# Optimization experiments

Measured on AMD Instinct MI355X. Metric: run time of the kernel, lower is better.

## Reference

```python
import jax, jax.numpy as jnp
import numpy as np

B, N, D, H = 2, 512, 384, 12
SQK, SV, PQ, PV = 16, 16, 4, 8
SCALE = 1.0 / np.sqrt(SQK + 4 * PQ)  # attention_scale, point_pair_dim=4
EPS = 1e-12


def setup_inputs() -> dict:
    key = jax.random.key(0)
    ks = jax.random.split(key, 10)

    def w(k, fan_in, fan_out):
        return (jax.random.normal(k, (fan_in, fan_out), jnp.float32) / np.sqrt(fan_in))

    return {
        "hidden": jax.random.normal(ks[0], (B, N, D), jnp.float32),
        "xyz": jax.random.normal(ks[1], (B, N, 3), jnp.float32),
        "W_qk": w(ks[2], D, 2 * H * SQK), "b_qk": jnp.zeros((2 * H * SQK,), jnp.float32),
        "W_vs": w(ks[3], D, H * SV), "b_vs": jnp.zeros((H * SV,), jnp.float32),
        "W_so": w(ks[4], H * SV, D), "b_so": jnp.zeros((D,), jnp.float32),
        "W_pqk": w(ks[5], D, H * PQ * 3), "b_pqk": jnp.zeros((H * PQ * 3,), jnp.float32),
        "W_pv": w(ks[6], D, H * PV * 3), "b_pv": jnp.zeros((H * PV * 3,), jnp.float32),
        "W_po": w(ks[7], H * PV * 3, D), "b_po": jnp.zeros((D,), jnp.float32),
        "W_fp": w(ks[8], 2 * D, D), "b_fp": jnp.zeros((D,), jnp.float32),
    }


def reference(hidden, xyz, W_qk, b_qk, W_vs, b_vs, W_so, b_so,
              W_pqk, b_pqk, W_pv, b_pv, W_po, b_po, W_fp, b_fp):
    # scalar q/k/v (note: heads are NOT split in the attention matmuls, per source)
    qk = hidden @ W_qk + b_qk                       # [B,N,2*H*SQK]
    q_s, k_s = jnp.split(qk, 2, axis=-1)            # [B,N,H*SQK] each
    v_s = hidden @ W_vs + b_vs                      # [B,N,H*SV]

    # points; k_points = q_points in source
    qp = (hidden @ W_pqk + b_pqk).reshape(B, N, H, PQ, 3)
    vp = hidden @ W_pv + b_pv                       # [B,N,H*PV*3]

    scalar_attn = jnp.einsum('bid,bjd->bij', q_s, k_s)  # [B,N,N]

    # fused pairwise point features: dist(q_i, k_j) + sum of 3 cosine components
    # = dist + cos_sim, per (head, point); avoid materializing [B,N,N,H,P,3].
    dot = jnp.einsum('bihpc,bjhpc->bijhp', qp, qp)      # [B,N,N,H,PQ]
    n2 = jnp.sum(qp * qp, axis=-1)                      # [B,N,H,PQ]
    d2 = n2[:, :, None] + n2[:, None] - 2.0 * dot
    dist = jnp.sqrt(jnp.maximum(d2, 0.0) + EPS)
    nrm = jnp.sqrt(n2 + EPS)
    cos = dot / (nrm[:, :, None] * nrm[:, None])
    point_attn = jnp.sum(dist + cos, axis=(-1, -2))     # [B,N,N]

    attn = jax.nn.softmax((scalar_attn + point_attn) * SCALE, axis=-1)

    scalar_result = jnp.einsum('bij,bjd->bid', attn, v_s)   # [B,N,H*SV]
    point_result = jnp.einsum('bij,bjd->bid', attn, vp)     # [B,N,H*PV*3]

    scalar_result = scalar_result @ W_so + b_so             # [B,N,D]
    point_result = point_result @ W_po + b_po               # [B,N,D]

    result = jnp.concatenate([scalar_result, point_result], axis=-1) @ W_fp + b_fp
    delta_xyz = point_result.reshape(B, N, -1, 3).mean(axis=2)  # [B,N,3]
    return result, xyz + delta_xyz
```

## Files before the change

kernel.cpp:

```cpp
#include <hip/hip_runtime.h>
#include <math.h>

typedef unsigned short u16;
typedef __attribute__((ext_vector_type(8))) short bf16x8;
typedef __attribute__((ext_vector_type(4))) float f32x4;

#define BB 2
#define NN 512
#define SCALEF 0.17677669529663687f

__device__ __forceinline__ u16 f2bf(float x) {
  union { float f; unsigned u; } c; c.f = x;
  unsigned r = (c.u + 0x7FFFu + ((c.u >> 16) & 1u)) >> 16;
  return (u16)r;
}
__device__ __forceinline__ float bf2f(u16 h) {
  union { unsigned u; float f; } c; c.u = ((unsigned)h) << 16;
  return c.f;
}
__device__ __forceinline__ void pack8(const float* v, bf16x8& h, bf16x8& l) {
#pragma unroll
  for (int j = 0; j < 8; ++j) {
    u16 hi = f2bf(v[j]);
    h[j] = (short)hi;
    l[j] = (short)f2bf(v[j] - bf2f(hi));
  }
}
#define MFMA3(ACC, AH, AL, BH, BL)                                              \
  ACC = __builtin_amdgcn_mfma_f32_16x16x32_bf16(AH, BH, ACC, 0, 0, 0);          \
  ACC = __builtin_amdgcn_mfma_f32_16x16x32_bf16(AH, BL, ACC, 0, 0, 0);          \
  ACC = __builtin_amdgcn_mfma_f32_16x16x32_bf16(AL, BH, ACC, 0, 0, 0);

template<int MR, int NF>
__device__ __forceinline__ void mfma_tile(
    const u16* __restrict__ Ah, const u16* __restrict__ Al, int lda,
    const u16* __restrict__ Bh, const u16* __restrict__ Bl, int ldb,
    int kBeg, int kEnd, int arow, int bcol, f32x4 (&acc)[MR][NF]) {
  const int lane = threadIdx.x & 63;
  const int rr = lane & 15, kg = lane >> 4;
  const u16* pah = Ah + (size_t)(arow + rr) * lda + kg * 8;
  const u16* pal = Al + (size_t)(arow + rr) * lda + kg * 8;
  const u16* pbh = Bh + (size_t)(bcol + rr) * ldb + kg * 8;
  const u16* pbl = Bl + (size_t)(bcol + rr) * ldb + kg * 8;
#pragma unroll 2
  for (int k0 = kBeg; k0 < kEnd; k0 += 32) {
    bf16x8 a_h[MR], a_l[MR], b_h[NF], b_l[NF];
#pragma unroll
    for (int m = 0; m < MR; ++m) {
      a_h[m] = *(const bf16x8*)(pah + (size_t)m * 16 * lda + k0);
      a_l[m] = *(const bf16x8*)(pal + (size_t)m * 16 * lda + k0);
    }
#pragma unroll
    for (int f = 0; f < NF; ++f) {
      b_h[f] = *(const bf16x8*)(pbh + (size_t)f * 16 * ldb + k0);
      b_l[f] = *(const bf16x8*)(pbl + (size_t)f * 16 * ldb + k0);
    }
#pragma unroll
    for (int m = 0; m < MR; ++m)
#pragma unroll
      for (int f = 0; f < NF; ++f) { MFMA3(acc[m][f], a_h[m], a_l[m], b_h[f], b_l[f]) }
  }
}

__global__ __launch_bounds__(512) void k_input(
    const float* __restrict__ hidden,
    const float* __restrict__ W_qk, const float* __restrict__ b_qk,
    const float* __restrict__ W_vs, const float* __restrict__ b_vs,
    const float* __restrict__ W_pv, const float* __restrict__ b_pv,
    const float* __restrict__ W_pqk, const float* __restrict__ b_pqk,
    const float* __restrict__ W_so, const float* __restrict__ b_so,
    const float* __restrict__ W_po, const float* __restrict__ b_po,
    const float* __restrict__ W_fp, const float* __restrict__ b_fp,
    u16* __restrict__ QKh, u16* __restrict__ QKl,
    u16* __restrict__ VTh, u16* __restrict__ VTl,
    float* __restrict__ QPf,
    u16* __restrict__ WCTh, u16* __restrict__ WCTl,
    float* __restrict__ bc, float* __restrict__ Wdf) {
  const int tid = threadIdx.x;
  if (blockIdx.x >= 21) {
    const int cx = blockIdx.x - 21, ky = blockIdx.y;
    if (ky < 10) {
      const int w = tid >> 6, lane = tid & 63;
      if (w >= 3) return;
      const int rr = lane & 15, kg = lane >> 4;
      const int c0 = cx * 48;
      const int kbase = ky * 48 + w * 16;
      const float* Wop; int moff;
      if (kbase < 192) { Wop = W_so + (size_t)kbase * 384; moff = 0; }
      else             { Wop = W_po + (size_t)(kbase - 192) * 384; moff = 384; }
      f32x4 acc[3] = {};
      const float* pa = Wop + (size_t)rr * 384 + kg * 8;
      const float* pw = W_fp + (size_t)moff * 384 + c0 + rr;
      for (int m0 = 0; m0 < 384; m0 += 32) {
        bf16x8 a_h, a_l, b_h[3], b_l[3];
        float v[8];
        *(float4*)&v[0] = *(const float4*)(pa + m0);
        *(float4*)&v[4] = *(const float4*)(pa + m0 + 4);
        pack8(v, a_h, a_l);
        const float* bp0 = pw + (size_t)(m0 + kg * 8) * 384;
#pragma unroll
        for (int f = 0; f < 3; ++f) {
          float u[8];
#pragma unroll
          for (int j = 0; j < 8; ++j) u[j] = bp0[(size_t)j * 384 + f * 16];
          pack8(u, b_h[f], b_l[f]);
        }
#pragma unroll
        for (int f = 0; f < 3; ++f) { MFMA3(acc[f], a_h, a_l, b_h[f], b_l[f]) }
      }
      const int rb = (lane >> 4) << 2, cc = lane & 15;
#pragma unroll
      for (int f = 0; f < 3; ++f) {
        int c = c0 + f * 16 + cc;
#pragma unroll
        for (int r = 0; r < 4; ++r) {
          int k = kbase + rb + r;
          float vv = acc[f][r];
          u16 hi = f2bf(vv);
          WCTh[(size_t)c * 480 + k] = hi;
          WCTl[(size_t)c * 480 + k] = f2bf(vv - bf2f(hi));
        }
      }
      return;
    }
    if (ky == 10) {
      const int colL = tid >> 3, part = tid & 7;
      if (colL >= 48) return;
      const int col = cx * 48 + colL;
      const float* bv = (part < 4) ? b_so : b_po;
      const int m0 = (part & 3) * 96;
      const float* wrow = W_fp + (size_t)part * 96 * 384 + col;
      float s0 = 0.f, s1 = 0.f, s2 = 0.f, s3 = 0.f;
#pragma unroll
      for (int i = 0; i < 96; i += 4) {
        s0 += bv[m0 + i]     * wrow[(size_t)(i)     * 384];
        s1 += bv[m0 + i + 1] * wrow[(size_t)(i + 1) * 384];
        s2 += bv[m0 + i + 2] * wrow[(size_t)(i + 2) * 384];
        s3 += bv[m0 + i + 3] * wrow[(size_t)(i + 3) * 384];
      }
      float s = (s0 + s1) + (s2 + s3);
      s += __shfl_down(s, 4, 8);
      s += __shfl_down(s, 2, 8);
      s += __shfl_down(s, 1, 8);
      if (part == 0) bc[col] = s + b_fp[col];
      return;
    }
    if (ky == 11) {
      const int out = tid >> 2, part = tid & 3;
      if (out < 108) {
        const int j = cx * 36 + out / 3, c = out - (out / 3) * 3;
        const float* src = W_po + (size_t)j * 384 + c + (size_t)part * 96;
        float s0 = 0.f, s1 = 0.f;
#pragma unroll
        for (int kk = 0; kk < 32; kk += 2) {
          s0 += src[3 * kk];
          s1 += src[3 * kk + 3];
        }
        float s = s0 + s1;
        s += __shfl_down(s, 2, 4);
        s += __shfl_down(s, 1, 4);
        if (part == 0) Wdf[j * 3 + c] = s * (1.0f / 128.f);
      } else if (cx == 0 && tid >= 432 && tid < 480) {
        int g = tid - 432, c = g >> 4, k0 = g & 15;
        float s = 0.f;
#pragma unroll
        for (int kk = 0; kk < 8; ++kk) s += b_po[3 * (k0 * 8 + kk) + c];
        for (int d = 8; d; d >>= 1) s += __shfl_down(s, d, 16);
        if (k0 == 0) Wdf[864 + c] = s * (1.0f / 128.f);
      }
      return;
    }
    return;
  }

  __shared__ f32x4 CB[7][2][3][64];
  __shared__ u16 Dh[48][32], Dl[48][32];
  const int w = tid >> 6, lane = tid & 63;
  const int rr = lane & 15, kg = lane >> 4;
  const int row0 = blockIdx.y * 32, col0 = blockIdx.x * 48;

  const float* W; const float* bias; int Ns, region;
  if (col0 < 384)      { W = W_qk;  Ns = 384; bias = b_qk + col0;          W += col0;       region = 0; }
  else if (col0 < 576) { W = W_vs;  Ns = 192; bias = b_vs + (col0 - 384);  W += col0 - 384; region = 1; }
  else if (col0 < 864) { W = W_pv;  Ns = 288; bias = b_pv + (col0 - 576);  W += col0 - 576; region = 1; }
  else                 { W = W_pqk; Ns = 144; bias = b_pqk + (col0 - 864); W += col0 - 864; region = 2; }

  f32x4 acc[2][3] = {};
  const float* pa = hidden + (size_t)(row0 + rr) * 384 + kg * 8;
  const float* pw = W + rr;
  for (int k0 = w * 32; k0 < 384; k0 += 256) {
    bf16x8 a_h[2], a_l[2], b_h[3], b_l[3];
#pragma unroll
    for (int m = 0; m < 2; ++m) {
      float v[8];
      *(float4*)&v[0] = *(const float4*)(pa + (size_t)m * 16 * 384 + k0);
      *(float4*)&v[4] = *(const float4*)(pa + (size_t)m * 16 * 384 + k0 + 4);
      pack8(v, a_h[m], a_l[m]);
    }
    const float* bp0 = pw + (size_t)(k0 + kg * 8) * Ns;
#pragma unroll
    for (int f = 0; f < 3; ++f) {
      float v[8];
#pragma unroll
      for (int j = 0; j < 8; ++j) v[j] = bp0[(size_t)j * Ns + f * 16];
      pack8(v, b_h[f], b_l[f]);
    }
#pragma unroll
    for (int m = 0; m < 2; ++m)
#pragma unroll
      for (int f = 0; f < 3; ++f) { MFMA3(acc[m][f], a_h[m], a_l[m], b_h[f], b_l[f]) }
  }
  if (w) {
#pragma unroll
    for (int m = 0; m < 2; ++m)
#pragma unroll
      for (int f = 0; f < 3; ++f) CB[w - 1][m][f][lane] = acc[m][f];
  }
  __syncthreads();
  if (w) return;
#pragma unroll
  for (int wv = 0; wv < 7; ++wv)
#pragma unroll
    for (int m = 0; m < 2; ++m)
#pragma unroll
      for (int f = 0; f < 3; ++f) acc[m][f] += CB[wv][m][f][lane];

  const int rb = (lane >> 4) << 2, cc = lane & 15;
  if (region == 0) {
#pragma unroll
    for (int f = 0; f < 3; ++f) {
      int n = col0 + f * 16 + cc;
      float bv = bias[f * 16 + cc];
#pragma unroll
      for (int m = 0; m < 2; ++m)
#pragma unroll
        for (int r = 0; r < 4; ++r) {
          float v = acc[m][f][r] + bv;
          int row = row0 + m * 16 + rb + r;
          u16 hi = f2bf(v);
          QKh[(size_t)row * 384 + n] = hi;
          QKl[(size_t)row * 384 + n] = f2bf(v - bf2f(hi));
        }
    }
  } else if (region == 2) {
#pragma unroll
    for (int f = 0; f < 3; ++f) {
      int c = (col0 - 864) + f * 16 + cc;
      float bv = bias[f * 16 + cc];
#pragma unroll
      for (int m = 0; m < 2; ++m)
#pragma unroll
        for (int r = 0; r < 4; ++r)
          QPf[(size_t)(row0 + m * 16 + rb + r) * 144 + c] = acc[m][f][r] + bv;
    }
  } else {
#pragma unroll
    for (int f = 0; f < 3; ++f) {
      float bv = bias[f * 16 + cc];
#pragma unroll
      for (int m = 0; m < 2; ++m)
#pragma unroll
        for (int r = 0; r < 4; ++r) {
          float v = acc[m][f][r] + bv;
          u16 hi = f2bf(v);
          Dh[f * 16 + cc][m * 16 + rb + r] = hi;
          Dl[f * 16 + cc][m * 16 + rb + r] = f2bf(v - bf2f(hi));
        }
    }
    const int b = row0 >> 9, rl = row0 & 511;
    const int cbase = col0 - 384;
    u16* dsth = VTh + (size_t)b * 480 * 512;
    u16* dstl = VTl + (size_t)b * 480 * 512;
    for (int u = lane; u < 192; u += 64) {
      int c = u >> 2, seg = u & 3;
      *(uint4*)(dsth + (size_t)(cbase + c) * 512 + rl + seg * 8) = *(const uint4*)&Dh[c][seg * 8];
      *(uint4*)(dstl + (size_t)(cbase + c) * 512 + rl + seg * 8) = *(const uint4*)&Dl[c][seg * 8];
    }
  }
}

#define PROW 244
__global__ __launch_bounds__(512) void k_attn(
    const u16* __restrict__ QKh, const u16* __restrict__ QKl,
    const float* __restrict__ QPf, float* __restrict__ ATTf) {
  __shared__ float Pi[32][PROW];
  __shared__ float Pj[32][PROW];
  __shared__ float Sf[2][32 * 33];
  const int b = blockIdx.z;
  int t = blockIdx.x, ti_ = 0;
  while (t >= 16 - ti_) { t -= 16 - ti_; ++ti_; }
  const int tj_ = ti_ + t;
  const int i0 = ti_ * 32, j0 = tj_ * 32;
  const bool offdiag = (tj_ != ti_);
  const int tid = threadIdx.x;
  for (int u = tid; u < 3072; u += 512) {
    int side = (u >= 1536) ? 1 : 0;
    int rem = u - side * 1536;
    int row = rem / 48, hp = rem - row * 48;
    int grow = b * NN + (side ? j0 : i0) + row;
    const float* p = QPf + (size_t)grow * 144 + hp * 3;
    float x = p[0], y = p[1], z = p[2];
    float n2 = x * x + y * y + z * z;
    float inv = __frsqrt_rn(n2 + 1e-12f);
    float* dst = side ? &Pj[row][0] : &Pi[row][0];
    ((float4*)dst)[hp] = make_float4(x, y, z, n2);
    dst[192 + hp] = inv;
  }
  __syncthreads();
  const int h = tid >> 8;
  const int t8 = tid & 255;
  const int tj = t8 & 15, ti = t8 >> 4;
  {
    float a00 = 0.f, a01 = 0.f, a10 = 0.f, a11 = 0.f;
    const float4* A0 = (const float4*)&Pi[ti][0];
    const float4* A1 = (const float4*)&Pi[ti + 16][0];
    const float4* B0 = (const float4*)&Pj[tj][0];
    const float4* B1 = (const float4*)&Pj[tj + 16][0];
    const float* iA0 = &Pi[ti][192];
    const float* iA1 = &Pi[ti + 16][192];
    const float* iB0 = &Pj[tj][192];
    const float* iB1 = &Pj[tj + 16][192];
    const int hpB = h * 24, hpE = hpB + 24;
#pragma unroll 4
    for (int hp = hpB; hp < hpE; ++hp) {
      float4 p0 = A0[hp], p1 = A1[hp], q0 = B0[hp], q1 = B1[hp];
      float va0 = iA0[hp], va1 = iA1[hp], vb0 = iB0[hp], vb1 = iB1[hp];
      {
        float dot = p0.x * q0.x + p0.y * q0.y + p0.z * q0.z;
        float d2 = fmaxf(fmaf(-2.f, dot, p0.w + q0.w), 0.f) + 1e-12f;
        a00 += d2 * __frsqrt_rn(d2) + dot * (va0 * vb0);
      }
      {
        float dot = p0.x * q1.x + p0.y * q1.y + p0.z * q1.z;
        float d2 = fmaxf(fmaf(-2.f, dot, p0.w + q1.w), 0.f) + 1e-12f;
        a01 += d2 * __frsqrt_rn(d2) + dot * (va0 * vb1);
      }
      {
        float dot = p1.x * q0.x + p1.y * q0.y + p1.z * q0.z;
        float d2 = fmaxf(fmaf(-2.f, dot, p1.w + q0.w), 0.f) + 1e-12f;
        a10 += d2 * __frsqrt_rn(d2) + dot * (va1 * vb0);
      }
      {
        float dot = p1.x * q1.x + p1.y * q1.y + p1.z * q1.z;
        float d2 = fmaxf(fmaf(-2.f, dot, p1.w + q1.w), 0.f) + 1e-12f;
        a11 += d2 * __frsqrt_rn(d2) + dot * (va1 * vb1);
      }
    }
    Sf[h][ti * 33 + tj] = a00;
    Sf[h][ti * 33 + tj + 16] = a01;
    Sf[h][(ti + 16) * 33 + tj] = a10;
    Sf[h][(ti + 16) * 33 + tj + 16] = a11;
  }
  const int w = tid >> 6, lane = tid & 63;
  const int dir = w >> 2, sub = w & 3;
  f32x4 q[1][1] = {};
  if (dir == 0) {
    int arow = b * NN + i0 + (sub >> 1) * 16;
    int brow = b * NN + j0 + (sub & 1) * 16;
    mfma_tile<1, 1>(QKh, QKl, 384, QKh + 192, QKl + 192, 384, 0, 192, arow, brow, q);
  } else if (offdiag) {
    int arow = b * NN + j0 + (sub >> 1) * 16;
    int brow = b * NN + i0 + (sub & 1) * 16;
    mfma_tile<1, 1>(QKh, QKl, 384, QKh + 192, QKl + 192, 384, 0, 192, arow, brow, q);
  }
  __syncthreads();
  const int rl = (sub >> 1) * 16 + ((lane >> 4) << 2);
  const int cl = (sub & 1) * 16 + (lane & 15);
  float* Cb = ATTf + (size_t)b * NN * NN;
  if (dir == 0) {
#pragma unroll
    for (int r = 0; r < 4; ++r)
      Cb[(size_t)(i0 + rl + r) * NN + j0 + cl] =
          q[0][0][r] + Sf[0][(rl + r) * 33 + cl] + Sf[1][(rl + r) * 33 + cl];
  } else if (offdiag) {
#pragma unroll
    for (int r = 0; r < 4; ++r)
      Cb[(size_t)(j0 + rl + r) * NN + i0 + cl] =
          q[0][0][r] + Sf[0][cl * 33 + rl + r] + Sf[1][cl * 33 + rl + r];
  }
}

__global__ __launch_bounds__(512) void k_pv(
    const float* __restrict__ ATTf,
    const u16* __restrict__ VTh, const u16* __restrict__ VTl,
    u16* __restrict__ SRh, u16* __restrict__ SRl) {
  __shared__ f32x4 CB[7][3][64];
  __shared__ float RS[7][64];
  const int tid = threadIdx.x;
  const int w = tid >> 6, lane = tid & 63;
  const int rr = lane & 15, kg = lane >> 4;
  const int b = blockIdx.z;
  const int row0 = blockIdx.y * 16, col0 = blockIdx.x * 48;
  const float* pa = ATTf + (size_t)(b * NN + row0 + rr) * NN + kg * 8;
  const u16* pbh = VTh + (size_t)b * 480 * 512 + (size_t)(col0 + rr) * 512 + kg * 8;
  const u16* pbl = VTl + (size_t)b * 480 * 512 + (size_t)(col0 + rr) * 512 + kg * 8;
  f32x4 acc[3] = {};
  float rs = 0.f;
  for (int k0 = w * 32; k0 < NN; k0 += 256) {
    bf16x8 a_h, a_l, b_h[3], b_l[3];
    {
      float v[8];
      *(float4*)&v[0] = *(const float4*)(pa + k0);
      *(float4*)&v[4] = *(const float4*)(pa + k0 + 4);
#pragma unroll
      for (int j = 0; j < 8; ++j) { float e = __expf(v[j] * SCALEF); rs += e; v[j] = e; }
      pack8(v, a_h, a_l);
    }
#pragma unroll
    for (int f = 0; f < 3; ++f) {
      b_h[f] = *(const bf16x8*)(pbh + (size_t)f * 16 * 512 + k0);
      b_l[f] = *(const bf16x8*)(pbl + (size_t)f * 16 * 512 + k0);
    }
#pragma unroll
    for (int f = 0; f < 3; ++f) { MFMA3(acc[f], a_h, a_l, b_h[f], b_l[f]) }
  }
  if (w) {
#pragma unroll
    for (int f = 0; f < 3; ++f) CB[w - 1][f][lane] = acc[f];
    RS[w - 1][lane] = rs;
  }
  __syncthreads();
  if (w) return;
#pragma unroll
  for (int wv = 0; wv < 7; ++wv) {
#pragma unroll
    for (int f = 0; f < 3; ++f) acc[f] += CB[wv][f][lane];
    rs += RS[wv][lane];
  }
  rs += __shfl_xor(rs, 16);
  rs += __shfl_xor(rs, 32);
  const int rb = (lane >> 4) << 2, cc = lane & 15;
  float inv[4];
#pragma unroll
  for (int r = 0; r < 4; ++r) inv[r] = 1.0f / __shfl(rs, rb + r);
  u16* oh = SRh + (size_t)b * NN * 480;
  u16* ol = SRl + (size_t)b * NN * 480;
#pragma unroll
  for (int f = 0; f < 3; ++f) {
    int n = col0 + f * 16 + cc;
#pragma unroll
    for (int r = 0; r < 4; ++r) {
      float v = acc[f][r] * inv[r];
      u16 hi = f2bf(v);
      oh[(size_t)(row0 + rb + r) * 480 + n] = hi;
      ol[(size_t)(row0 + rb + r) * 480 + n] = f2bf(v - bf2f(hi));
    }
  }
}

__global__ __launch_bounds__(512) void k_tail(
    const u16* __restrict__ SRh, const u16* __restrict__ SRl,
    const u16* __restrict__ WCTh, const u16* __restrict__ WCTl,
    const float* __restrict__ bc, const float* __restrict__ Wdf,
    const float* __restrict__ xyz,
    float* __restrict__ out_res, float* __restrict__ out_xyz) {
  const int tid = threadIdx.x;
  const int row0 = blockIdx.y * 16;
  if (blockIdx.x == 8) {
    if (tid < 384) {
      int out = tid >> 3, part = tid & 7;
      int lt = out / 3, c = out - lt * 3;
      int token = row0 + lt;
      const u16* sh = SRh + (size_t)token * 480 + 192 + part * 36;
      const u16* sl = SRl + (size_t)token * 480 + 192 + part * 36;
      float s = 0.f;
#pragma unroll 4
      for (int kk = 0; kk < 36; ++kk) {
        float v = bf2f(sh[kk]) + bf2f(sl[kk]);
        s += v * Wdf[(part * 36 + kk) * 3 + c];
      }
#pragma unroll
      for (int d = 4; d; d >>= 1) s += __shfl_down(s, d, 8);
      if (part == 0)
        out_xyz[(size_t)token * 3 + c] = xyz[(size_t)token * 3 + c] + s + Wdf[864 + c];
    }
    return;
  }
  __shared__ f32x4 CB[7][3][64];
  const int w = tid >> 6, lane = tid & 63;
  const int rr = lane & 15, kg = lane >> 4;
  const int col0 = blockIdx.x * 48;
  const u16* pah = SRh + (size_t)(row0 + rr) * 480 + kg * 8;
  const u16* pal = SRl + (size_t)(row0 + rr) * 480 + kg * 8;
  const u16* pbh = WCTh + (size_t)(col0 + rr) * 480 + kg * 8;
  const u16* pbl = WCTl + (size_t)(col0 + rr) * 480 + kg * 8;
  f32x4 acc[3] = {};
  for (int k0 = w * 32; k0 < 480; k0 += 256) {
    bf16x8 a_h, a_l, b_h[3], b_l[3];
    a_h = *(const bf16x8*)(pah + k0);
    a_l = *(const bf16x8*)(pal + k0);
#pragma unroll
    for (int f = 0; f < 3; ++f) {
      b_h[f] = *(const bf16x8*)(pbh + (size_t)f * 16 * 480 + k0);
      b_l[f] = *(const bf16x8*)(pbl + (size_t)f * 16 * 480 + k0);
    }
#pragma unroll
    for (int f = 0; f < 3; ++f) { MFMA3(acc[f], a_h, a_l, b_h[f], b_l[f]) }
  }
  if (w) {
#pragma unroll
    for (int f = 0; f < 3; ++f) CB[w - 1][f][lane] = acc[f];
  }
  __syncthreads();
  if (w) return;
#pragma unroll
  for (int wv = 0; wv < 7; ++wv)
#pragma unroll
    for (int f = 0; f < 3; ++f) acc[f] += CB[wv][f][lane];
  const int rb = (lane >> 4) << 2, cc = lane & 15;
#pragma unroll
  for (int f = 0; f < 3; ++f) {
    int n = col0 + f * 16 + cc;
#pragma unroll
    for (int r = 0; r < 4; ++r)
      out_res[(size_t)(row0 + rb + r) * 384 + n] = acc[f][r] + bc[n];
  }
}

extern "C" void kernel_launch(void* const* d_in, const int* in_sizes, int n_in,
                              void* d_out, int out_size, void* d_ws, size_t ws_size,
                              hipStream_t stream) {
  const float* hidden = (const float*)d_in[0];
  const float* xyz   = (const float*)d_in[1];
  const float* W_qk  = (const float*)d_in[2];
  const float* b_qk  = (const float*)d_in[3];
  const float* W_vs  = (const float*)d_in[4];
  const float* b_vs  = (const float*)d_in[5];
  const float* W_so  = (const float*)d_in[6];
  const float* b_so  = (const float*)d_in[7];
  const float* W_pqk = (const float*)d_in[8];
  const float* b_pqk = (const float*)d_in[9];
  const float* W_pv  = (const float*)d_in[10];
  const float* b_pv  = (const float*)d_in[11];
  const float* W_po  = (const float*)d_in[12];
  const float* b_po  = (const float*)d_in[13];
  const float* W_fp  = (const float*)d_in[14];
  const float* b_fp  = (const float*)d_in[15];

  float* out_res = (float*)d_out;
  float* out_xyz = out_res + (size_t)BB * NN * 384;

  u16* p   = (u16*)d_ws;
  u16* QKh  = p;           p += 393216;
  u16* QKl  = p;           p += 393216;
  u16* VTh  = p;           p += 491520;
  u16* VTl  = p;           p += 491520;
  u16* SRh  = p;           p += 491520;
  u16* SRl  = p;           p += 491520;
  u16* WCTh = p;           p += 184320;
  u16* WCTl = p;           p += 184320;
  float* QPf  = (float*)p; p += 2 * 147456;
  float* ATTf = (float*)p; p += 2 * 524288;
  float* bcf  = (float*)p; p += 2 * 384;
  float* Wdf  = (float*)p;

  k_input<<<dim3(29, 32), 512, 0, stream>>>(hidden,
                                            W_qk, b_qk, W_vs, b_vs, W_pv, b_pv, W_pqk, b_pqk,
                                            W_so, b_so, W_po, b_po, W_fp, b_fp,
                                            QKh, QKl, VTh, VTl, QPf, WCTh, WCTl, bcf, Wdf);
  k_attn<<<dim3(136, 1, 2), 512, 0, stream>>>(QKh, QKl, QPf, ATTf);
  k_pv<<<dim3(10, 32, 2), 512, 0, stream>>>(ATTf, VTh, VTl, SRh, SRl);
  k_tail<<<dim3(9, 64), 512, 0, stream>>>(SRh, SRl, WCTh, WCTl, bcf, Wdf, xyz,
                                          out_res, out_xyz);
}
```

Before: 65.52 us.

## Fold output projection into values before attention and merge into three kernels

Uses associativity to multiply the value matrix by the combined output weights (V·Wc) before the attention-weighted sum. That product is computed in extra blocks of the attention kernel, so the separate tail GEMM kernel and its intermediate buffer are gone. The PV kernel now writes final outputs directly, with softmax normalization and bias applied. The xyz delta is computed as the attention times a precomputed per-token projection. This removes one launch and one intermediate round trip to memory, at the cost of heavier attention-kernel blocks and different rounding order.

```diff
diff --git a/kernel.cpp b/kernel.cpp
--- a/kernel.cpp
+++ b/kernel.cpp
@@ -72,7 +72,7 @@
     const float* __restrict__ W_po, const float* __restrict__ b_po,
     const float* __restrict__ W_fp, const float* __restrict__ b_fp,
     u16* __restrict__ QKh, u16* __restrict__ QKl,
-    u16* __restrict__ VTh, u16* __restrict__ VTl,
+    u16* __restrict__ VRh, u16* __restrict__ VRl,
     float* __restrict__ QPf,
     u16* __restrict__ WCTh, u16* __restrict__ WCTl,
     float* __restrict__ bc, float* __restrict__ Wdf) {
@@ -174,7 +174,6 @@
   }
 
   __shared__ f32x4 CB[7][2][3][64];
-  __shared__ u16 Dh[48][32], Dl[48][32];
   const int w = tid >> 6, lane = tid & 63;
   const int rr = lane & 15, kg = lane >> 4;
   const int row0 = blockIdx.y * 32, col0 = blockIdx.x * 48;
@@ -256,43 +255,111 @@
   } else {
 #pragma unroll
     for (int f = 0; f < 3; ++f) {
+      int c = (col0 - 384) + f * 16 + cc;
       float bv = bias[f * 16 + cc];
 #pragma unroll
       for (int m = 0; m < 2; ++m)
 #pragma unroll
         for (int r = 0; r < 4; ++r) {
           float v = acc[m][f][r] + bv;
+          int row = row0 + m * 16 + rb + r;
           u16 hi = f2bf(v);
-          Dh[f * 16 + cc][m * 16 + rb + r] = hi;
-          Dl[f * 16 + cc][m * 16 + rb + r] = f2bf(v - bf2f(hi));
-        }
-    }
-    const int b = row0 >> 9, rl = row0 & 511;
-    const int cbase = col0 - 384;
-    u16* dsth = VTh + (size_t)b * 480 * 512;
-    u16* dstl = VTl + (size_t)b * 480 * 512;
-    for (int u = lane; u < 192; u += 64) {
-      int c = u >> 2, seg = u & 3;
-      *(uint4*)(dsth + (size_t)(cbase + c) * 512 + rl + seg * 8) = *(const uint4*)&Dh[c][seg * 8];
-      *(uint4*)(dstl + (size_t)(cbase + c) * 512 + rl + seg * 8) = *(const uint4*)&Dl[c][seg * 8];
-    }
-  }
-}
-
-#define PROW 244
+          VRh[(size_t)row * 480 + c] = hi;
+          VRl[(size_t)row * 480 + c] = f2bf(v - bf2f(hi));
+        }
+    }
+  }
+}
+
 __global__ __launch_bounds__(512) void k_attn(
     const u16* __restrict__ QKh, const u16* __restrict__ QKl,
-    const float* __restrict__ QPf, float* __restrict__ ATTf) {
-  __shared__ float Pi[32][PROW];
-  __shared__ float Pj[32][PROW];
-  __shared__ float Sf[2][32 * 33];
+    const float* __restrict__ QPf,
+    const u16* __restrict__ VRh, const u16* __restrict__ VRl,
+    const u16* __restrict__ WCTh, const u16* __restrict__ WCTl,
+    const float* __restrict__ Wdf,
+    float* __restrict__ ATTf, u16* __restrict__ VCTh, u16* __restrict__ VCTl,
+    float* __restrict__ VCdT) {
+  __shared__ __align__(16) char smem[70912];
+  const int tid = threadIdx.x;
   const int b = blockIdx.z;
+  if (blockIdx.x >= 136) {
+    const int xx = blockIdx.x - 136;
+    if (xx < 256) {
+      f32x4 (*CB)[3][64] = (f32x4 (*)[3][64])smem;
+      u16 (*Dh)[16] = (u16 (*)[16])(smem + 21504);
+      u16 (*Dl)[16] = (u16 (*)[16])(smem + 23040);
+      const int tile = xx >> 3, cx = xx & 7;
+      const int row0 = tile * 16, c0 = cx * 48;
+      const int w = tid >> 6, lane = tid & 63;
+      const int rr = lane & 15, kg = lane >> 4;
+      const u16* pah = VRh + (size_t)(b * NN + row0 + rr) * 480 + kg * 8;
+      const u16* pal = VRl + (size_t)(b * NN + row0 + rr) * 480 + kg * 8;
+      const u16* pbh = WCTh + (size_t)(c0 + rr) * 480 + kg * 8;
+      const u16* pbl = WCTl + (size_t)(c0 + rr) * 480 + kg * 8;
+      f32x4 acc[3] = {};
+      for (int k0 = w * 32; k0 < 480; k0 += 256) {
+        bf16x8 a_h, a_l, b_h[3], b_l[3];
+        a_h = *(const bf16x8*)(pah + k0);
+        a_l = *(const bf16x8*)(pal + k0);
+#pragma unroll
+        for (int f = 0; f < 3; ++f) {
+          b_h[f] = *(const bf16x8*)(pbh + (size_t)f * 16 * 480 + k0);
+          b_l[f] = *(const bf16x8*)(pbl + (size_t)f * 16 * 480 + k0);
+        }
+#pragma unroll
+        for (int f = 0; f < 3; ++f) { MFMA3(acc[f], a_h, a_l, b_h[f], b_l[f]) }
+      }
+      if (w) {
+#pragma unroll
+        for (int f = 0; f < 3; ++f) CB[w - 1][f][lane] = acc[f];
+      }
+      __syncthreads();
+      if (w) return;
+#pragma unroll
+      for (int wv = 0; wv < 7; ++wv)
+#pragma unroll
+        for (int f = 0; f < 3; ++f) acc[f] += CB[wv][f][lane];
+      const int rb = (lane >> 4) << 2, cc = lane & 15;
+#pragma unroll
+      for (int f = 0; f < 3; ++f)
+#pragma unroll
+        for (int r = 0; r < 4; ++r) {
+          float v = acc[f][r];
+          u16 hi = f2bf(v);
+          Dh[f * 16 + cc][rb + r] = hi;
+          Dl[f * 16 + cc][rb + r] = f2bf(v - bf2f(hi));
+        }
+      for (int u = lane; u < 192; u += 64) {
+        int col = u >> 2, rem = u & 3, hl = rem >> 1, chunk = rem & 1;
+        const u16* src = (hl ? Dl : Dh)[col] + chunk * 8;
+        u16* dst = (hl ? VCTl : VCTh) + ((size_t)b * 384 + c0 + col) * 512 + row0 + chunk * 8;
+        *(uint4*)dst = *(const uint4*)src;
+      }
+      return;
+    }
+    const int c = xx - 256;
+    float* WdL = (float*)smem;
+    for (int i = tid; i < 288; i += 512) WdL[i] = Wdf[i * 3 + c];
+    __syncthreads();
+    const u16* vh = VRh + (size_t)(b * NN + tid) * 480 + 192;
+    const u16* vl = VRl + (size_t)(b * NN + tid) * 480 + 192;
+    float s0 = 0.f, s1 = 0.f;
+#pragma unroll 4
+    for (int j = 0; j < 288; j += 2) {
+      s0 += (bf2f(vh[j]) + bf2f(vl[j])) * WdL[j];
+      s1 += (bf2f(vh[j + 1]) + bf2f(vl[j + 1])) * WdL[j + 1];
+    }
+    VCdT[((size_t)b * 3 + c) * 512 + tid] = s0 + s1;
+    return;
+  }
+  float (*Pi)[244] = (float (*)[244])smem;
+  float (*Pj)[244] = (float (*)[244])(smem + 31232);
+  float* Sf = (float*)(smem + 62464);
   int t = blockIdx.x, ti_ = 0;
   while (t >= 16 - ti_) { t -= 16 - ti_; ++ti_; }
   const int tj_ = ti_ + t;
   const int i0 = ti_ * 32, j0 = tj_ * 32;
   const bool offdiag = (tj_ != ti_);
-  const int tid = threadIdx.x;
   for (int u = tid; u < 3072; u += 512) {
     int side = (u >= 1536) ? 1 : 0;
     int rem = u - side * 1536;
@@ -346,10 +413,10 @@
         a11 += d2 * __frsqrt_rn(d2) + dot * (va1 * vb1);
       }
     }
-    Sf[h][ti * 33 + tj] = a00;
-    Sf[h][ti * 33 + tj + 16] = a01;
-    Sf[h][(ti + 16) * 33 + tj] = a10;
-    Sf[h][(ti + 16) * 33 + tj + 16] = a11;
+    Sf[h * 1056 + ti * 33 + tj] = a00;
+    Sf[h * 1056 + ti * 33 + tj + 16] = a01;
+    Sf[h * 1056 + (ti + 16) * 33 + tj] = a10;
+    Sf[h * 1056 + (ti + 16) * 33 + tj + 16] = a11;
   }
   const int w = tid >> 6, lane = tid & 63;
   const int dir = w >> 2, sub = w & 3;
@@ -371,29 +438,54 @@
 #pragma unroll
     for (int r = 0; r < 4; ++r)
       Cb[(size_t)(i0 + rl + r) * NN + j0 + cl] =
-          q[0][0][r] + Sf[0][(rl + r) * 33 + cl] + Sf[1][(rl + r) * 33 + cl];
+          q[0][0][r] + Sf[(rl + r) * 33 + cl] + Sf[1056 + (rl + r) * 33 + cl];
   } else if (offdiag) {
 #pragma unroll
     for (int r = 0; r < 4; ++r)
       Cb[(size_t)(j0 + rl + r) * NN + i0 + cl] =
-          q[0][0][r] + Sf[0][cl * 33 + rl + r] + Sf[1][cl * 33 + rl + r];
-  }
-}
-
-__global__ __launch_bounds__(512) void k_pv(
+          q[0][0][r] + Sf[cl * 33 + rl + r] + Sf[1056 + cl * 33 + rl + r];
+  }
+}
+
+__global__ __launch_bounds__(512) void k_pv_out(
     const float* __restrict__ ATTf,
-    const u16* __restrict__ VTh, const u16* __restrict__ VTl,
-    u16* __restrict__ SRh, u16* __restrict__ SRl) {
+    const u16* __restrict__ VCTh, const u16* __restrict__ VCTl,
+    const float* __restrict__ VCdT, const float* __restrict__ bc,
+    const float* __restrict__ Wdf, const float* __restrict__ xyz,
+    float* __restrict__ out_res, float* __restrict__ out_xyz) {
+  const int tid = threadIdx.x;
+  const int b = blockIdx.z;
+  const int row0 = blockIdx.y * 16;
+  if (blockIdx.x == 8) {
+    const int part = tid & 7, rest = tid >> 3;
+    const int c = rest % 3, lt = rest / 3;
+    if (lt < 16) {
+      const float* arow = ATTf + ((size_t)b * NN + row0 + lt) * NN + part * 64;
+      const float* vcd = VCdT + ((size_t)b * 3 + c) * 512 + part * 64;
+      float s = 0.f, rs = 0.f;
+#pragma unroll 8
+      for (int kk = 0; kk < 64; ++kk) {
+        float e = __expf(arow[kk] * SCALEF);
+        s += e * vcd[kk];
+        rs += e;
+      }
+#pragma unroll
+      for (int d = 4; d; d >>= 1) { s += __shfl_down(s, d, 8); rs += __shfl_down(rs, d, 8); }
+      if (part == 0) {
+        size_t idx = ((size_t)b * NN + row0 + lt) * 3 + c;
+        out_xyz[idx] = xyz[idx] + s / rs + Wdf[864 + c];
+      }
+    }
+    return;
+  }
   __shared__ f32x4 CB[7][3][64];
   __shared__ float RS[7][64];
-  const int tid = threadIdx.x;
   const int w = tid >> 6, lane = tid & 63;
   const int rr = lane & 15, kg = lane >> 4;
-  const int b = blockIdx.z;
-  const int row0 = blockIdx.y * 16, col0 = blockIdx.x * 48;
+  const int col0 = blockIdx.x * 48;
   const float* pa = ATTf + (size_t)(b * NN + row0 + rr) * NN + kg * 8;
-  const u16* pbh = VTh + (size_t)b * 480 * 512 + (size_t)(col0 + rr) * 512 + kg * 8;
-  const u16* pbl = VTl + (size_t)b * 480 * 512 + (size_t)(col0 + rr) * 512 + kg * 8;
+  const u16* pbh = VCTh + ((size_t)b * 384 + col0 + rr) * 512 + kg * 8;
+  const u16* pbl = VCTl + ((size_t)b * 384 + col0 + rr) * 512 + kg * 8;
   f32x4 acc[3] = {};
   float rs = 0.f;
   for (int k0 = w * 32; k0 < NN; k0 += 256) {
@@ -433,87 +525,13 @@
   float inv[4];
 #pragma unroll
   for (int r = 0; r < 4; ++r) inv[r] = 1.0f / __shfl(rs, rb + r);
-  u16* oh = SRh + (size_t)b * NN * 480;
-  u16* ol = SRl + (size_t)b * NN * 480;
 #pragma unroll
   for (int f = 0; f < 3; ++f) {
     int n = col0 + f * 16 + cc;
-#pragma unroll
-    for (int r = 0; r < 4; ++r) {
-      float v = acc[f][r] * inv[r];
-      u16 hi = f2bf(v);
-      oh[(size_t)(row0 + rb + r) * 480 + n] = hi;
-      ol[(size_t)(row0 + rb + r) * 480 + n] = f2bf(v - bf2f(hi));
-    }
-  }
-}
-
-__global__ __launch_bounds__(512) void k_tail(
-    const u16* __restrict__ SRh, const u16* __restrict__ SRl,
-    const u16* __restrict__ WCTh, const u16* __restrict__ WCTl,
-    const float* __restrict__ bc, const float* __restrict__ Wdf,
-    const float* __restrict__ xyz,
-    float* __restrict__ out_res, float* __restrict__ out_xyz) {
-  const int tid = threadIdx.x;
-  const int row0 = blockIdx.y * 16;
-  if (blockIdx.x == 8) {
-    if (tid < 384) {
-      int out = tid >> 3, part = tid & 7;
-      int lt = out / 3, c = out - lt * 3;
-      int token = row0 + lt;
-      const u16* sh = SRh + (size_t)token * 480 + 192 + part * 36;
-      const u16* sl = SRl + (size_t)token * 480 + 192 + part * 36;
-      float s = 0.f;
-#pragma unroll 4
-      for (int kk = 0; kk < 36; ++kk) {
-        float v = bf2f(sh[kk]) + bf2f(sl[kk]);
-        s += v * Wdf[(part * 36 + kk) * 3 + c];
-      }
-#pragma unroll
-      for (int d = 4; d; d >>= 1) s += __shfl_down(s, d, 8);
-      if (part == 0)
-        out_xyz[(size_t)token * 3 + c] = xyz[(size_t)token * 3 + c] + s + Wdf[864 + c];
-    }
-    return;
-  }
-  __shared__ f32x4 CB[7][3][64];
-  const int w = tid >> 6, lane = tid & 63;
-  const int rr = lane & 15, kg = lane >> 4;
-  const int col0 = blockIdx.x * 48;
-  const u16* pah = SRh + (size_t)(row0 + rr) * 480 + kg * 8;
-  const u16* pal = SRl + (size_t)(row0 + rr) * 480 + kg * 8;
-  const u16* pbh = WCTh + (size_t)(col0 + rr) * 480 + kg * 8;
-  const u16* pbl = WCTl + (size_t)(col0 + rr) * 480 + kg * 8;
-  f32x4 acc[3] = {};
-  for (int k0 = w * 32; k0 < 480; k0 += 256) {
-    bf16x8 a_h, a_l, b_h[3], b_l[3];
-    a_h = *(const bf16x8*)(pah + k0);
-    a_l = *(const bf16x8*)(pal + k0);
-#pragma unroll
-    for (int f = 0; f < 3; ++f) {
-      b_h[f] = *(const bf16x8*)(pbh + (size_t)f * 16 * 480 + k0);
-      b_l[f] = *(const bf16x8*)(pbl + (size_t)f * 16 * 480 + k0);
-    }
-#pragma unroll
-    for (int f = 0; f < 3; ++f) { MFMA3(acc[f], a_h, a_l, b_h[f], b_l[f]) }
-  }
-  if (w) {
-#pragma unroll
-    for (int f = 0; f < 3; ++f) CB[w - 1][f][lane] = acc[f];
-  }
-  __syncthreads();
-  if (w) return;
-#pragma unroll
-  for (int wv = 0; wv < 7; ++wv)
-#pragma unroll
-    for (int f = 0; f < 3; ++f) acc[f] += CB[wv][f][lane];
-  const int rb = (lane >> 4) << 2, cc = lane & 15;
-#pragma unroll
-  for (int f = 0; f < 3; ++f) {
-    int n = col0 + f * 16 + cc;
+    float bcv = bc[n];
 #pragma unroll
     for (int r = 0; r < 4; ++r)
-      out_res[(size_t)(row0 + rb + r) * 384 + n] = acc[f][r] + bc[n];
+      out_res[((size_t)b * NN + row0 + rb + r) * 384 + n] = acc[f][r] * inv[r] + bcv;
   }
 }
 
@@ -543,23 +561,25 @@
   u16* p   = (u16*)d_ws;
   u16* QKh  = p;           p += 393216;
   u16* QKl  = p;           p += 393216;
-  u16* VTh  = p;           p += 491520;
-  u16* VTl  = p;           p += 491520;
-  u16* SRh  = p;           p += 491520;
-  u16* SRl  = p;           p += 491520;
+  u16* VRh  = p;           p += 491520;
+  u16* VRl  = p;           p += 491520;
+  u16* VCTh = p;           p += 393216;
+  u16* VCTl = p;           p += 393216;
   u16* WCTh = p;           p += 184320;
   u16* WCTl = p;           p += 184320;
   float* QPf  = (float*)p; p += 2 * 147456;
   float* ATTf = (float*)p; p += 2 * 524288;
+  float* VCdT = (float*)p; p += 2 * 3072;
   float* bcf  = (float*)p; p += 2 * 384;
   float* Wdf  = (float*)p;
 
   k_input<<<dim3(29, 32), 512, 0, stream>>>(hidden,
                                             W_qk, b_qk, W_vs, b_vs, W_pv, b_pv, W_pqk, b_pqk,
                                             W_so, b_so, W_po, b_po, W_fp, b_fp,
-                                            QKh, QKl, VTh, VTl, QPf, WCTh, WCTl, bcf, Wdf);
-  k_attn<<<dim3(136, 1, 2), 512, 0, stream>>>(QKh, QKl, QPf, ATTf);
-  k_pv<<<dim3(10, 32, 2), 512, 0, stream>>>(ATTf, VTh, VTl, SRh, SRl);
-  k_tail<<<dim3(9, 64), 512, 0, stream>>>(SRh, SRl, WCTh, WCTl, bcf, Wdf, xyz,
-                                          out_res, out_xyz);
-}
+                                            QKh, QKl, VRh, VRl, QPf, WCTh, WCTl, bcf, Wdf);
+  k_attn<<<dim3(395, 1, 2), 512, 0, stream>>>(QKh, QKl, QPf, VRh, VRl,
+                                              WCTh, WCTl, Wdf,
+                                              ATTf, VCTh, VCTl, VCdT);
+  k_pv_out<<<dim3(9, 32, 2), 512, 0, stream>>>(ATTf, VCTh, VCTl, VCdT, bcf, Wdf, xyz,
+                                               out_res, out_xyz);
+}
```

Result: slower. 72.70 us (+11.0%).

## Fuse P·V and output projection into one kernel via shared memory

Applied to the files above, without the earlier changes.

Merges the softmax·V kernel and the tail projection kernel into a single kernel. Each block handles 16 rows, keeps the exponentiated attention row tile and the intermediate result in LDS, and removes the global SR buffers and one kernel launch. In exchange the grid drops from 640 and 576 blocks to 64, which lowers parallelism and occupancy. Each block also now streams the full V and W matrices with no split-K across waves.

```diff
diff --git a/kernel.cpp b/kernel.cpp
--- a/kernel.cpp
+++ b/kernel.cpp
@@ -380,140 +380,110 @@
   }
 }
 
-__global__ __launch_bounds__(512) void k_pv(
+#define PLD 520
+#define SLD 488
+__global__ __launch_bounds__(512) void k_pv_tail(
     const float* __restrict__ ATTf,
     const u16* __restrict__ VTh, const u16* __restrict__ VTl,
-    u16* __restrict__ SRh, u16* __restrict__ SRl) {
-  __shared__ f32x4 CB[7][3][64];
-  __shared__ float RS[7][64];
-  const int tid = threadIdx.x;
-  const int w = tid >> 6, lane = tid & 63;
-  const int rr = lane & 15, kg = lane >> 4;
-  const int b = blockIdx.z;
-  const int row0 = blockIdx.y * 16, col0 = blockIdx.x * 48;
-  const float* pa = ATTf + (size_t)(b * NN + row0 + rr) * NN + kg * 8;
-  const u16* pbh = VTh + (size_t)b * 480 * 512 + (size_t)(col0 + rr) * 512 + kg * 8;
-  const u16* pbl = VTl + (size_t)b * 480 * 512 + (size_t)(col0 + rr) * 512 + kg * 8;
-  f32x4 acc[3] = {};
-  float rs = 0.f;
-  for (int k0 = w * 32; k0 < NN; k0 += 256) {
-    bf16x8 a_h, a_l, b_h[3], b_l[3];
-    {
-      float v[8];
-      *(float4*)&v[0] = *(const float4*)(pa + k0);
-      *(float4*)&v[4] = *(const float4*)(pa + k0 + 4);
-#pragma unroll
-      for (int j = 0; j < 8; ++j) { float e = __expf(v[j] * SCALEF); rs += e; v[j] = e; }
-      pack8(v, a_h, a_l);
-    }
-#pragma unroll
-    for (int f = 0; f < 3; ++f) {
-      b_h[f] = *(const bf16x8*)(pbh + (size_t)f * 16 * 512 + k0);
-      b_l[f] = *(const bf16x8*)(pbl + (size_t)f * 16 * 512 + k0);
-    }
-#pragma unroll
-    for (int f = 0; f < 3; ++f) { MFMA3(acc[f], a_h, a_l, b_h[f], b_l[f]) }
-  }
-  if (w) {
-#pragma unroll
-    for (int f = 0; f < 3; ++f) CB[w - 1][f][lane] = acc[f];
-    RS[w - 1][lane] = rs;
-  }
-  __syncthreads();
-  if (w) return;
-#pragma unroll
-  for (int wv = 0; wv < 7; ++wv) {
-#pragma unroll
-    for (int f = 0; f < 3; ++f) acc[f] += CB[wv][f][lane];
-    rs += RS[wv][lane];
-  }
-  rs += __shfl_xor(rs, 16);
-  rs += __shfl_xor(rs, 32);
-  const int rb = (lane >> 4) << 2, cc = lane & 15;
-  float inv[4];
-#pragma unroll
-  for (int r = 0; r < 4; ++r) inv[r] = 1.0f / __shfl(rs, rb + r);
-  u16* oh = SRh + (size_t)b * NN * 480;
-  u16* ol = SRl + (size_t)b * NN * 480;
-#pragma unroll
-  for (int f = 0; f < 3; ++f) {
-    int n = col0 + f * 16 + cc;
-#pragma unroll
-    for (int r = 0; r < 4; ++r) {
-      float v = acc[f][r] * inv[r];
-      u16 hi = f2bf(v);
-      oh[(size_t)(row0 + rb + r) * 480 + n] = hi;
-      ol[(size_t)(row0 + rb + r) * 480 + n] = f2bf(v - bf2f(hi));
-    }
-  }
-}
-
-__global__ __launch_bounds__(512) void k_tail(
-    const u16* __restrict__ SRh, const u16* __restrict__ SRl,
     const u16* __restrict__ WCTh, const u16* __restrict__ WCTl,
     const float* __restrict__ bc, const float* __restrict__ Wdf,
     const float* __restrict__ xyz,
     float* __restrict__ out_res, float* __restrict__ out_xyz) {
+  __shared__ u16 Ph[16][PLD], Pl[16][PLD];
+  __shared__ u16 Sh[16][SLD], Sl[16][SLD];
+  __shared__ float rsL[16];
   const int tid = threadIdx.x;
-  const int row0 = blockIdx.y * 16;
-  if (blockIdx.x == 8) {
-    if (tid < 384) {
-      int out = tid >> 3, part = tid & 7;
-      int lt = out / 3, c = out - lt * 3;
-      int token = row0 + lt;
-      const u16* sh = SRh + (size_t)token * 480 + 192 + part * 36;
-      const u16* sl = SRl + (size_t)token * 480 + 192 + part * 36;
-      float s = 0.f;
-#pragma unroll 4
-      for (int kk = 0; kk < 36; ++kk) {
-        float v = bf2f(sh[kk]) + bf2f(sl[kk]);
-        s += v * Wdf[(part * 36 + kk) * 3 + c];
-      }
-#pragma unroll
-      for (int d = 4; d; d >>= 1) s += __shfl_down(s, d, 8);
-      if (part == 0)
-        out_xyz[(size_t)token * 3 + c] = xyz[(size_t)token * 3 + c] + s + Wdf[864 + c];
-    }
-    return;
-  }
-  __shared__ f32x4 CB[7][3][64];
+  const int b = blockIdx.z;
+  const int row0 = blockIdx.x * 16;
+
+  {
+    const int r = tid >> 5, cg = tid & 31;
+    const float* arow = ATTf + ((size_t)(b * NN + row0 + r)) * NN + cg * 16;
+    float part = 0.f;
+#pragma unroll
+    for (int q = 0; q < 16; q += 4) {
+      float4 v = *(const float4*)(arow + q);
+      float e0 = __expf(v.x * SCALEF), e1 = __expf(v.y * SCALEF);
+      float e2 = __expf(v.z * SCALEF), e3 = __expf(v.w * SCALEF);
+      part += (e0 + e1) + (e2 + e3);
+      u16 h0 = f2bf(e0), h1 = f2bf(e1), h2 = f2bf(e2), h3 = f2bf(e3);
+      *(ushort4*)&Ph[r][cg * 16 + q] = make_ushort4(h0, h1, h2, h3);
+      *(ushort4*)&Pl[r][cg * 16 + q] = make_ushort4(
+          f2bf(e0 - bf2f(h0)), f2bf(e1 - bf2f(h1)),
+          f2bf(e2 - bf2f(h2)), f2bf(e3 - bf2f(h3)));
+    }
+#pragma unroll
+    for (int d = 16; d; d >>= 1) part += __shfl_down(part, d, 32);
+    if (cg == 0) rsL[r] = part;
+  }
+  __syncthreads();
+
   const int w = tid >> 6, lane = tid & 63;
   const int rr = lane & 15, kg = lane >> 4;
-  const int col0 = blockIdx.x * 48;
-  const u16* pah = SRh + (size_t)(row0 + rr) * 480 + kg * 8;
-  const u16* pal = SRl + (size_t)(row0 + rr) * 480 + kg * 8;
-  const u16* pbh = WCTh + (size_t)(col0 + rr) * 480 + kg * 8;
-  const u16* pbl = WCTl + (size_t)(col0 + rr) * 480 + kg * 8;
-  f32x4 acc[3] = {};
-  for (int k0 = w * 32; k0 < 480; k0 += 256) {
-    bf16x8 a_h, a_l, b_h[3], b_l[3];
-    a_h = *(const bf16x8*)(pah + k0);
-    a_l = *(const bf16x8*)(pal + k0);
-#pragma unroll
-    for (int f = 0; f < 3; ++f) {
-      b_h[f] = *(const bf16x8*)(pbh + (size_t)f * 16 * 480 + k0);
-      b_l[f] = *(const bf16x8*)(pbl + (size_t)f * 16 * 480 + k0);
-    }
-#pragma unroll
-    for (int f = 0; f < 3; ++f) { MFMA3(acc[f], a_h, a_l, b_h[f], b_l[f]) }
-  }
-  if (w) {
-#pragma unroll
-    for (int f = 0; f < 3; ++f) CB[w - 1][f][lane] = acc[f];
+  const int rb = (lane >> 4) << 2, cc = lane & 15;
+  float invr[4];
+#pragma unroll
+  for (int r = 0; r < 4; ++r) invr[r] = 1.0f / rsL[rb + r];
+
+  const u16* vbh = VTh + (size_t)b * 480 * 512;
+  const u16* vbl = VTl + (size_t)b * 480 * 512;
+  for (int nf = w; nf < 30; nf += 8) {
+    f32x4 acc = {0.f, 0.f, 0.f, 0.f};
+    const u16* pbh = vbh + (size_t)(nf * 16 + rr) * 512 + kg * 8;
+    const u16* pbl = vbl + (size_t)(nf * 16 + rr) * 512 + kg * 8;
+#pragma unroll 4
+    for (int k0 = 0; k0 < 512; k0 += 32) {
+      bf16x8 a_h = *(const bf16x8*)&Ph[rr][k0 + kg * 8];
+      bf16x8 a_l = *(const bf16x8*)&Pl[rr][k0 + kg * 8];
+      bf16x8 b_h = *(const bf16x8*)(pbh + k0);
+      bf16x8 b_l = *(const bf16x8*)(pbl + k0);
+      MFMA3(acc, a_h, a_l, b_h, b_l)
+    }
+#pragma unroll
+    for (int r = 0; r < 4; ++r) {
+      float v = acc[r] * invr[r];
+      u16 hi = f2bf(v);
+      Sh[rb + r][nf * 16 + cc] = hi;
+      Sl[rb + r][nf * 16 + cc] = f2bf(v - bf2f(hi));
+    }
   }
   __syncthreads();
-  if (w) return;
-#pragma unroll
-  for (int wv = 0; wv < 7; ++wv)
-#pragma unroll
-    for (int f = 0; f < 3; ++f) acc[f] += CB[wv][f][lane];
-  const int rb = (lane >> 4) << 2, cc = lane & 15;
-#pragma unroll
-  for (int f = 0; f < 3; ++f) {
-    int n = col0 + f * 16 + cc;
+
+  for (int nf = w; nf < 24; nf += 8) {
+    f32x4 acc = {0.f, 0.f, 0.f, 0.f};
+    const u16* pbh = WCTh + (size_t)(nf * 16 + rr) * 480 + kg * 8;
+    const u16* pbl = WCTl + (size_t)(nf * 16 + rr) * 480 + kg * 8;
+#pragma unroll 3
+    for (int k0 = 0; k0 < 480; k0 += 32) {
+      bf16x8 a_h = *(const bf16x8*)&Sh[rr][k0 + kg * 8];
+      bf16x8 a_l = *(const bf16x8*)&Sl[rr][k0 + kg * 8];
+      bf16x8 b_h = *(const bf16x8*)(pbh + k0);
+      bf16x8 b_l = *(const bf16x8*)(pbl + k0);
+      MFMA3(acc, a_h, a_l, b_h, b_l)
+    }
+    int n = nf * 16 + cc;
+    float bcv = bc[n];
 #pragma unroll
     for (int r = 0; r < 4; ++r)
-      out_res[(size_t)(row0 + rb + r) * 384 + n] = acc[f][r] + bc[n];
+      out_res[((size_t)(b * NN + row0 + rb + r)) * 384 + n] = acc[r] + bcv;
+  }
+
+  if (tid < 384) {
+    const int part = tid & 7, rest = tid >> 3;
+    const int c = rest % 3, lt = rest / 3;
+    const u16* sh = &Sh[lt][192 + part * 36];
+    const u16* sl = &Sl[lt][192 + part * 36];
+    const float* wd = Wdf + (part * 36) * 3 + c;
+    float s = 0.f;
+#pragma unroll 4
+    for (int kk = 0; kk < 36; ++kk)
+      s += (bf2f(sh[kk]) + bf2f(sl[kk])) * wd[kk * 3];
+#pragma unroll
+    for (int d = 4; d; d >>= 1) s += __shfl_down(s, d, 8);
+    if (part == 0) {
+      size_t idx = ((size_t)(b * NN + row0 + lt)) * 3 + c;
+      out_xyz[idx] = xyz[idx] + s + Wdf[864 + c];
+    }
   }
 }
 
@@ -545,8 +515,6 @@
   u16* QKl  = p;           p += 393216;
   u16* VTh  = p;           p += 491520;
   u16* VTl  = p;           p += 491520;
-  u16* SRh  = p;           p += 491520;
-  u16* SRl  = p;           p += 491520;
   u16* WCTh = p;           p += 184320;
   u16* WCTl = p;           p += 184320;
   float* QPf  = (float*)p; p += 2 * 147456;
@@ -559,7 +527,6 @@
                                             W_so, b_so, W_po, b_po, W_fp, b_fp,
                                             QKh, QKl, VTh, VTl, QPf, WCTh, WCTl, bcf, Wdf);
   k_attn<<<dim3(136, 1, 2), 512, 0, stream>>>(QKh, QKl, QPf, ATTf);
-  k_pv<<<dim3(10, 32, 2), 512, 0, stream>>>(ATTf, VTh, VTl, SRh, SRl);
-  k_tail<<<dim3(9, 64), 512, 0, stream>>>(SRh, SRl, WCTh, WCTl, bcf, Wdf, xyz,
-                                          out_res, out_xyz);
-}
+  k_pv_tail<<<dim3(32, 1, 2), 512, 0, stream>>>(ATTf, VTh, VTl, WCTh, WCTl,
+                                                bcf, Wdf, xyz, out_res, out_xyz);
+}
```

Result: slower. 87.33 us (+33.3%).
